# Optimization experiments

Hardware: AMD Instinct MI355X
Metric: run time of the kernel (lower is better)

Reference implementation:

```python
import jax, jax.numpy as jnp
import numpy as np

# ---- fixed problem dimensions ----
B, S, T = 64, 200, 32          # batch of sequences, trees per seq, nodes per tree
V, E, C = 50000, 128, 128      # vocab, embedding_dim, encode_dim
H, OUT = 100, 104              # GRU hidden, output_dim
N = B * S * T                  # total nodes
D_MAX = 5                      # max depth of a 32-node complete binary tree


def setup_inputs() -> dict:
    key = jax.random.key(0)
    ks = jax.random.split(key, 16)
    # --- tree structure: every tree is a complete binary tree with T nodes ---
    local_parent = np.array([0] + [(i - 1) // 2 for i in range(1, T)], dtype=np.int64)
    local_depth = np.array([int(np.floor(np.log2(i + 1))) for i in range(T)], dtype=np.int64)
    num_trees = B * S
    offsets = np.arange(num_trees, dtype=np.int64) * T
    node_parent = (offsets[:, None] + local_parent[None, :]).reshape(-1)
    node_depth = np.tile(local_depth, num_trees)
    node_tree = np.repeat(np.arange(num_trees, dtype=np.int64), T)
    node_tokens = jax.random.randint(ks[0], (N,), 0, V, dtype=jnp.int64)
    sc = 0.05
    inp = {
        "node_tokens": node_tokens,
        "node_parent": jnp.asarray(node_parent),
        "node_tree": jnp.asarray(node_tree),
        "node_depth": jnp.asarray(node_depth),
        "emb": jax.random.normal(ks[1], (V, E), jnp.float32) * sc,
        "w_lin": jax.random.normal(ks[2], (C, E), jnp.float32) * sc,
        "b_lin": jnp.zeros((C,), jnp.float32),
        "w_ih_f": jax.random.normal(ks[3], (3 * H, C), jnp.float32) * sc,
        "w_hh_f": jax.random.normal(ks[4], (3 * H, H), jnp.float32) * sc,
        "b_ih_f": jnp.zeros((3 * H,), jnp.float32),
        "b_hh_f": jnp.zeros((3 * H,), jnp.float32),
        "w_ih_b": jax.random.normal(ks[5], (3 * H, C), jnp.float32) * sc,
        "w_hh_b": jax.random.normal(ks[6], (3 * H, H), jnp.float32) * sc,
        "b_ih_b": jnp.zeros((3 * H,), jnp.float32),
        "b_hh_b": jnp.zeros((3 * H,), jnp.float32),
        "fc_w": jax.random.normal(ks[7], (OUT, 2 * H), jnp.float32) * sc,
        "fc_b": jnp.zeros((OUT,), jnp.float32),
    }
    return inp


def _gru(x_sbc, w_ih, w_hh, b_ih, b_hh):
    """Torch-convention GRU over leading time axis. x_sbc: [S, B, C] -> [S, B, H]."""
    h0 = jnp.zeros((x_sbc.shape[1], w_hh.shape[1]), x_sbc.dtype)

    def step(h, xt):
        gx = xt @ w_ih.T + b_ih
        gh = h @ w_hh.T + b_hh
        xr, xz, xn = jnp.split(gx, 3, axis=-1)
        hr, hz, hn = jnp.split(gh, 3, axis=-1)
        r = jax.nn.sigmoid(xr + hr)
        z = jax.nn.sigmoid(xz + hz)
        n = jnp.tanh(xn + r * hn)
        h_new = (1.0 - z) * n + z * h
        return h_new, h_new

    _, hs = jax.lax.scan(step, h0, x_sbc)
    return hs


def reference(node_tokens, node_parent, node_tree, node_depth,
              emb, w_lin, b_lin,
              w_ih_f, w_hh_f, b_ih_f, b_hh_f,
              w_ih_b, w_hh_b, b_ih_b, b_hh_b,
              fc_w, fc_b):
    # per-node contribution: W * emb(token) + b   (recursion base of hidden_state)
    c = emb[node_tokens] @ w_lin.T + b_lin               # [N, C]
    # level-batched bottom-up scatter-add: h(node) = c(node) + sum(h(children))
    h = c
    for d in range(D_MAX, 0, -1):
        mask = (node_depth == d)[:, None]
        h = h.at[node_parent].add(jnp.where(mask, h, 0.0))
    # per-tree max pool over all node hidden states (TreeEncoder output)
    tree_vec = jax.ops.segment_max(h, node_tree, num_segments=B * S)  # [B*S, C]
    x = tree_vec.reshape(B, S, C)
    # bidirectional GRU (batch_first in torch; scan over time here)
    x_t = jnp.transpose(x, (1, 0, 2))                    # [S, B, C]
    fwd = _gru(x_t, w_ih_f, w_hh_f, b_ih_f, b_hh_f)      # [S, B, H]
    bwd = _gru(x_t[::-1], w_ih_b, w_hh_b, b_ih_b, b_hh_b)[::-1]
    gru_out = jnp.concatenate([fwd, bwd], axis=-1)       # [S, B, 2H]
    pool = gru_out.max(axis=0)                           # [B, 2H] (max over time)
    return pool @ fc_w.T + fc_b                          # [B, OUT]
```

## Files before the change

kernel.cpp:

```cpp
#include <hip/hip_runtime.h>
#include <hip/hip_bf16.h>
#include <math.h>

#define BB 64
#define SS 200
#define TT 32
#define VV 50000
#define EE 128
#define CC 128
#define HH 100
#define G3 300
#define OUTD 104
#define NTREE (BB*SS)

typedef __attribute__((ext_vector_type(4))) float f32x4;
typedef _Float16 f16x8 __attribute__((ext_vector_type(8)));

#define L2E  1.4426950408889634f
#define NL2E (-1.4426950408889634f)
#define TL2E 2.8853900817779268f

#define BAR() asm volatile("s_waitcnt lgkmcnt(0)\n\ts_barrier" ::: "memory")


__global__ __launch_bounds__(256) void k0_prep(const float* __restrict__ w_lin,
                                               const float* __restrict__ w_ih_f,
                                               const float* __restrict__ w_ih_b,
                                               const float* __restrict__ w_hh_f,
                                               const float* __restrict__ w_hh_b,
                                               const float* __restrict__ emb,
                                               _Float16* __restrict__ wl,
                                               _Float16* __restrict__ k2b,
                                               _Float16* __restrict__ k3b,
                                               _Float16* __restrict__ emb16) {
    const int tid  = threadIdx.x;
    const int wave = tid >> 6;
    const int lane = tid & 63;
    const int r = lane & 15;
    const int q = lane >> 4;
    if (blockIdx.x == 0) {
#pragma unroll
        for (int nt = 0; nt < 2; ++nt)
#pragma unroll
            for (int kt = 0; kt < 4; ++kt) {
                const int n = wave * 32 + nt * 16 + r;
                const float* src = w_lin + (long)n * EE + kt * 32 + q * 8;
                f16x8 f;
#pragma unroll
                for (int e = 0; e < 8; ++e) f[e] = (_Float16)src[e];
                *(f16x8*)&wl[(size_t)((((wave * 2 + nt) * 4 + kt) * 64) + lane) * 8] = f;
            }
    } else if (blockIdx.x <= 10) {
        const int nb = blockIdx.x - 1;
        const int n = nb * 64 + wave * 16 + r;
        const int dir = (n >= 320) ? 1 : 0;
        const int j = n - dir * 320;
        const int jj = (j < G3) ? j : 0;
        const float* w = dir ? w_ih_b : w_ih_f;
#pragma unroll
        for (int kt = 0; kt < 4; ++kt) {
            const float* src = w + (long)jj * EE + kt * 32 + q * 8;
            f16x8 f;
#pragma unroll
            for (int e = 0; e < 8; ++e) f[e] = (_Float16)src[e];
            *(f16x8*)&k2b[(size_t)((((nb * 4 + wave) * 4 + kt) * 64) + lane) * 8] = f;
        }
    } else if (blockIdx.x <= 12) {
        const int d = blockIdx.x - 11;
        const float* whh = d ? w_hh_b : w_hh_f;
#pragma unroll
        for (int t = 0; t < 6; ++t) {
            const int gate = (t < 3) ? t : t - 3;
            const int ch   = (t < 3) ? r : 16 + r;
            const bool nv  = (ch < 25);
            const int row  = gate * HH + wave * 25 + (nv ? ch : 0);
            const float sc = (gate == 2) ? TL2E : NL2E;
#pragma unroll
            for (int kt = 0; kt < 4; ++kt) {
                f16x8 f;
#pragma unroll
                for (int e = 0; e < 8; ++e) {
                    const int k = kt * 32 + q * 8 + e;
                    f[e] = (_Float16)((nv && k < HH) ? sc * whh[row * HH + k] : 0.f);
                }
                *(f16x8*)&k3b[(size_t)((((d * 4 + wave) * 6 + t) * 4 + kt) * 64 + lane) * 8] = f;
            }
        }
    } else {
        const long base = (long)(blockIdx.x - 13) * 2048 + (long)tid * 8;
        if (base < (long)VV * EE) {
            const float4* s = (const float4*)(emb + base);
            const float4 v0 = s[0], v1 = s[1];
            f16x8 f;
            f[0] = (_Float16)v0.x; f[1] = (_Float16)v0.y;
            f[2] = (_Float16)v0.z; f[3] = (_Float16)v0.w;
            f[4] = (_Float16)v1.x; f[5] = (_Float16)v1.y;
            f[6] = (_Float16)v1.z; f[7] = (_Float16)v1.w;
            *(f16x8*)&emb16[base] = f;
        }
    }
}

#define K1_TPI 2
#define AROWS (K1_TPI*TT)
#define LDA 136
#define LDC 132

__global__ __launch_bounds__(256) void k1_mfma(const int* __restrict__ tok,
                                               const _Float16* __restrict__ emb16,
                                               const _Float16* __restrict__ wl,
                                               const float* __restrict__ b_lin,
                                               _Float16* __restrict__ thi) {
    __shared__ __align__(16) _Float16 A_sh[AROWS * LDA];
    __shared__ __align__(16) float C_sh[AROWS * LDC];
    __shared__ int tok_sh[AROWS];

    const int tid  = threadIdx.x;
    const int wave = tid >> 6;
    const int lane = tid & 63;
    const int r = lane & 15;
    const int q = lane >> 4;

    f16x8 bfrag[2][4];
    float bias[2];
#pragma unroll
    for (int nt = 0; nt < 2; ++nt) {
        bias[nt] = b_lin[wave * 32 + nt * 16 + r];
#pragma unroll
        for (int kt = 0; kt < 4; ++kt)
            bfrag[nt][kt] = *(const f16x8*)&wl[(size_t)((((wave * 2 + nt) * 4 + kt) * 64) + lane) * 8];
    }

    const int tree0 = blockIdx.x * K1_TPI;
    if (tid < AROWS) tok_sh[tid] = tok[tree0 * TT + tid];
    __syncthreads();

#pragma unroll
    for (int i = 0; i < 4; ++i) {
        const int idx = tid + i * 256;
        const int row = idx >> 4;
        const int p   = idx & 15;
        const f16x8 v = *(const f16x8*)&emb16[(long)tok_sh[row] * EE + p * 8];
        *(f16x8*)&A_sh[row * LDA + p * 8] = v;
    }
    __syncthreads();

    f32x4 acc[4][2];
#pragma unroll
    for (int mt = 0; mt < 4; ++mt)
#pragma unroll
        for (int nt = 0; nt < 2; ++nt) acc[mt][nt] = (f32x4)(0.f);

#pragma unroll
    for (int mt = 0; mt < 4; ++mt) {
        const int m = mt * 16 + r;
        f16x8 afrag[4];
#pragma unroll
        for (int kt = 0; kt < 4; ++kt)
            afrag[kt] = *(const f16x8*)&A_sh[m * LDA + kt * 32 + q * 8];
#pragma unroll
        for (int nt = 0; nt < 2; ++nt)
#pragma unroll
            for (int kt = 0; kt < 4; ++kt)
                acc[mt][nt] = __builtin_amdgcn_mfma_f32_16x16x32_f16(
                    afrag[kt], bfrag[nt][kt], acc[mt][nt], 0, 0, 0);
    }

#pragma unroll
    for (int mt = 0; mt < 4; ++mt)
#pragma unroll
        for (int nt = 0; nt < 2; ++nt) {
            const int col = wave * 32 + nt * 16 + r;
#pragma unroll
            for (int reg = 0; reg < 4; ++reg) {
                const int row = mt * 16 + q * 4 + reg;
                C_sh[row * LDC + col] = acc[mt][nt][reg] + bias[nt];
            }
        }
    __syncthreads();

    {
        const int t = tid >> 7;
        const int j = tid & 127;
        const float* base = &C_sh[(t * TT) * LDC + j];
        float v[TT];
#pragma unroll
        for (int n = 0; n < TT; ++n) v[n] = base[n * LDC];
        float mx = -1e30f;
#pragma unroll
        for (int n = TT - 1; n >= 1; --n) {
            mx = fmaxf(mx, v[n]);
            v[(n - 1) >> 1] += v[n];
        }
        mx = fmaxf(mx, v[0]);
        thi[(size_t)(tree0 + t) * CC + j] = (_Float16)mx;
    }
}

__global__ __launch_bounds__(256) void k2_mfma(const _Float16* __restrict__ thi,
                                               const _Float16* __restrict__ k2b,
                                               const float* __restrict__ b_ih_f,
                                               const float* __restrict__ b_ih_b,
                                               float* __restrict__ gx) {
    __shared__ __align__(16) _Float16 Ah[32 * LDA];

    const int tid  = threadIdx.x;
    const int wave = tid >> 6;
    const int lane = tid & 63;
    const int r = lane & 15;
    const int q = lane >> 4;

    const int nb = blockIdx.x % 10;
    const int mb = blockIdx.x / 10;
    const int m0 = mb * 32;
    const int n0 = nb * 64;

#pragma unroll
    for (int i = 0; i < 2; ++i) {
        const int idx = tid + i * 256;
        const int row = idx >> 4;
        const int p   = idx & 15;
        f16x8 v = *(const f16x8*)&thi[(size_t)(m0 + row) * CC + p * 8];
        *(f16x8*)&Ah[row * LDA + p * 8] = v;
    }
    f16x8 bh[4];
#pragma unroll
    for (int kt = 0; kt < 4; ++kt)
        bh[kt] = *(const f16x8*)&k2b[(size_t)((((nb * 4 + wave) * 4 + kt) * 64) + lane) * 8];
    __syncthreads();

    f32x4 acc[2];
    acc[0] = (f32x4)(0.f); acc[1] = (f32x4)(0.f);
#pragma unroll
    for (int mt = 0; mt < 2; ++mt) {
        const int m = mt * 16 + r;
#pragma unroll
        for (int kt = 0; kt < 4; ++kt) {
            f16x8 a = *(const f16x8*)&Ah[m * LDA + kt * 32 + q * 8];
            acc[mt] = __builtin_amdgcn_mfma_f32_16x16x32_f16(a, bh[kt], acc[mt], 0, 0, 0);
        }
    }

    const int ng  = n0 + wave * 16 + r;
    const int dir = (ng >= 320) ? 1 : 0;
    const int j   = ng - dir * 320;
    const bool valid = (j < G3);
    const float bias = valid ? (dir ? b_ih_b[j] : b_ih_f[j]) : 0.f;
    float* gxd = gx + (long)dir * NTREE * G3;
    if (valid) {
#pragma unroll
        for (int mt = 0; mt < 2; ++mt)
#pragma unroll
            for (int reg = 0; reg < 4; ++reg) {
                const int m = m0 + mt * 16 + q * 4 + reg;
                gxd[(long)m * G3 + j] = acc[mt][reg] + bias;
            }
    }
}

__global__ __launch_bounds__(256, 1) void k3_gru(const float* __restrict__ gx,
                                                 const _Float16* __restrict__ k3b,
                                                 const float* __restrict__ b_hh_f,
                                                 const float* __restrict__ b_hh_b,
                                                 float* __restrict__ pool) {
    const int bid = blockIdx.x;
    const int dir = bid & 1;
    const int b   = bid >> 1;
    const int tid = threadIdx.x;
    const int wave = tid >> 6;
    const int lane = tid & 63;
    const int r = lane & 15;
    const int q = lane >> 4;

    const float* b_hh = dir ? b_hh_b : b_hh_f;

    __shared__ __align__(16) _Float16 h_sh[2][128];

    const int dw = dir * 4 + wave;
    f16x8 bf[6][4];
#pragma unroll
    for (int t = 0; t < 6; ++t)
#pragma unroll
        for (int kt = 0; kt < 4; ++kt)
            bf[t][kt] = *(const f16x8*)&k3b[(size_t)(((dw * 6 + t) * 4 + kt) * 64 + lane) * 8];

    const int m = lane;
    const int c = wave * 25 + m;
    const bool act  = (m < 25);
    const bool lo16 = (m < 16);
    float brc = 0.f, bzc = 0.f, bnc = 0.f;
    if (act) {
        brc = NL2E * b_hh[c];
        bzc = NL2E * b_hh[HH + c];
        bnc = TL2E * b_hh[2 * HH + c];
    }

    if (tid < 128) { h_sh[0][tid] = (_Float16)0.f; h_sh[1][tid] = (_Float16)0.f; }

    const int sstep = dir ? -1 : 1;
    const int s0 = dir ? (SS - 1) : 0;
    const float* gp = gx + (long)dir * NTREE * G3 + (long)b * SS * G3 + c;

    float pxr[4], pxz[4], pxn[4];
    if (act) {
#pragma unroll
        for (int j = 0; j < 4; ++j) {
            const long off = (long)(s0 + j * sstep) * G3;
            pxr[j] = gp[off]; pxz[j] = gp[off + HH]; pxn[j] = gp[off + 2 * HH];
        }
    }
    float hj = 0.f, hmax = -1e30f;
    __syncthreads();

    int s = s0;
    for (int t0 = 0; t0 < SS; t0 += 4) {
#pragma unroll
        for (int j = 0; j < 4; ++j) {
            const int p = j & 1;

            f16x8 a[4];
#pragma unroll
            for (int kt = 0; kt < 4; ++kt)
                a[kt] = *(const f16x8*)&h_sh[p][kt * 32 + q * 8];

            const float xr = __builtin_fmaf(pxr[j], NL2E, brc);
            const float xz = __builtin_fmaf(pxz[j], NL2E, bzc);
            const float xn = pxn[j] * TL2E;

            f32x4 accA[6], accB[6];
#pragma unroll
            for (int i = 0; i < 6; ++i) {
                accA[i] = (f32x4)(0.f);
                accB[i] = (f32x4)(0.f);
                accA[i] = __builtin_amdgcn_mfma_f32_16x16x32_f16(a[0], bf[i][0], accA[i], 0, 0, 0);
                accB[i] = __builtin_amdgcn_mfma_f32_16x16x32_f16(a[2], bf[i][2], accB[i], 0, 0, 0);
                accA[i] = __builtin_amdgcn_mfma_f32_16x16x32_f16(a[1], bf[i][1], accA[i], 0, 0, 0);
                accB[i] = __builtin_amdgcn_mfma_f32_16x16x32_f16(a[3], bf[i][3], accB[i], 0, 0, 0);
            }
            const float G0 = accA[0][0] + accB[0][0];
            const float G1 = accA[1][0] + accB[1][0];
            const float G2 = accA[2][0] + accB[2][0];
            const float G3v = accA[3][0] + accB[3][0];
            const float G4 = accA[4][0] + accB[4][0];
            const float G5 = accA[5][0] + accB[5][0];
            const float ghr = lo16 ? G0 : G3v;
            const float ghz = lo16 ? G1 : G4;
            const float ghn = lo16 ? G2 : G5;

            if (act) {
                const float rg = __builtin_amdgcn_rcpf(1.f + __builtin_amdgcn_exp2f(xr + ghr));
                const float zg = __builtin_amdgcn_rcpf(1.f + __builtin_amdgcn_exp2f(xz + ghz));
                const float t1 = ghn + bnc;
                const float an = __builtin_fmaf(rg, t1, xn);
                const float u  = __builtin_amdgcn_rcpf(1.f + __builtin_amdgcn_exp2f(an));
                const float n  = __builtin_fmaf(-2.f, u, 1.f);
                hj = __builtin_fmaf(zg, hj - n, n);
                h_sh[1 - p][c] = (_Float16)hj;
                hmax = fmaxf(hmax, hj);
                if (t0 + j + 4 < SS) {
                    const long off = (long)(s + (j + 4) * sstep) * G3;
                    pxr[j] = gp[off]; pxz[j] = gp[off + HH]; pxn[j] = gp[off + 2 * HH];
                }
            }
            BAR();
        }
        s += 4 * sstep;
    }
    if (act) pool[(long)b * (2 * HH) + dir * HH + c] = hmax;
}

__global__ __launch_bounds__(256) void k4_fc(const float* __restrict__ pool,
                                             const float* __restrict__ fc_w,
                                             const float* __restrict__ fc_b,
                                             float* __restrict__ out) {
    const int b = blockIdx.x;
    __shared__ __align__(16) float p_sh[2 * HH];
    const int t = threadIdx.x;
    if (t < 2 * HH) p_sh[t] = pool[(long)b * (2 * HH) + t];
    __syncthreads();
    if (t < OUTD) {
        const float4* wr4 = (const float4*)(fc_w + (long)t * (2 * HH));
        const float4* p4 = (const float4*)p_sh;
        float a0 = 0.f, a1 = 0.f;
#pragma unroll
        for (int k = 0; k < 50; k += 2) {
            float4 w0 = wr4[k],   p0 = p4[k];
            float4 w1 = wr4[k+1], p1 = p4[k+1];
            a0 += w0.x*p0.x + w0.y*p0.y + w0.z*p0.z + w0.w*p0.w;
            a1 += w1.x*p1.x + w1.y*p1.y + w1.z*p1.z + w1.w*p1.w;
        }
        out[(long)b * OUTD + t] = fc_b[t] + a0 + a1;
    }
}

extern "C" void kernel_launch(void* const* d_in, const int* in_sizes, int n_in,
                              void* d_out, int out_size, void* d_ws, size_t ws_size,
                              hipStream_t stream) {
    const int*   tok    = (const int*)d_in[0];
    const float* emb    = (const float*)d_in[4];
    const float* w_lin  = (const float*)d_in[5];
    const float* b_lin  = (const float*)d_in[6];
    const float* w_ih_f = (const float*)d_in[7];
    const float* w_hh_f = (const float*)d_in[8];
    const float* b_ih_f = (const float*)d_in[9];
    const float* b_hh_f = (const float*)d_in[10];
    const float* w_ih_b = (const float*)d_in[11];
    const float* w_hh_b = (const float*)d_in[12];
    const float* b_ih_b = (const float*)d_in[13];
    const float* b_hh_b = (const float*)d_in[14];
    const float* fc_w   = (const float*)d_in[15];
    const float* fc_b   = (const float*)d_in[16];

    char* wsb = (char*)d_ws;
    _Float16* wl    = (_Float16*)(wsb);
    _Float16* k2b   = (_Float16*)(wsb + 32768);
    _Float16* thi   = (_Float16*)(wsb + 196608);
    _Float16* k3b   = (_Float16*)(wsb + 3473408);
    float*    gx    = (float*)(wsb + 3670016);
    _Float16* emb16 = (_Float16*)(wsb + 3670016);
    float*    pool  = (float*)(wsb);
    float*    out   = (float*)d_out;

    k0_prep<<<13 + 3125, 256, 0, stream>>>(w_lin, w_ih_f, w_ih_b, w_hh_f, w_hh_b, emb,
                                           wl, k2b, k3b, emb16);
    k1_mfma<<<NTREE / K1_TPI, 256, 0, stream>>>(tok, emb16, wl, b_lin, thi);
    k2_mfma<<<(NTREE / 32) * 10, 256, 0, stream>>>(thi, k2b, b_ih_f, b_ih_b, gx);
    k3_gru <<<2 * BB, 256, 0, stream>>>(gx, k3b, b_hh_f, b_hh_b, pool);
    k4_fc  <<<BB, 256, 0, stream>>>(pool, fc_w, fc_b, out);
}
```

Baseline: 252.5 us.

## Batch 16 sequences per GRU block so recurrent MFMAs use all rows

The GRU recurrence kernel previously ran one sequence per block (128 blocks), with each MFMA using only one of its 16 rows. It now processes 16 batch rows per block (8 blocks total), with the weights as the A operand and the hidden states of 16 sequences as the B operand, so each MFMA does useful work across all rows. The r/z hidden biases and the log2 scaling are folded into the gx projection kernel, and the LDS hidden-state buffer is XOR-swizzled. In exchange, far fewer CUs are occupied, and each of the 200 serial steps carries more MFMA and transcendental work per wave, so the latency-bound loop may lengthen.

```diff
diff --git a/kernel.cpp b/kernel.cpp
--- a/kernel.cpp
+++ b/kernel.cpp
@@ -15,6 +15,7 @@
 
 typedef __attribute__((ext_vector_type(4))) float f32x4;
 typedef _Float16 f16x8 __attribute__((ext_vector_type(8)));
+typedef _Float16 f16x4 __attribute__((ext_vector_type(4)));
 
 #define L2E  1.4426950408889634f
 #define NL2E (-1.4426950408889634f)
@@ -31,7 +32,7 @@
                                                const float* __restrict__ emb,
                                                _Float16* __restrict__ wl,
                                                _Float16* __restrict__ k2b,
-                                               _Float16* __restrict__ k3b,
+                                               _Float16* __restrict__ k3c,
                                                _Float16* __restrict__ emb16) {
     const int tid  = threadIdx.x;
     const int wave = tid >> 6;
@@ -68,23 +69,19 @@
     } else if (blockIdx.x <= 12) {
         const int d = blockIdx.x - 11;
         const float* whh = d ? w_hh_b : w_hh_f;
-#pragma unroll
-        for (int t = 0; t < 6; ++t) {
-            const int gate = (t < 3) ? t : t - 3;
-            const int ch   = (t < 3) ? r : 16 + r;
-            const bool nv  = (ch < 25);
-            const int row  = gate * HH + wave * 25 + (nv ? ch : 0);
-            const float sc = (gate == 2) ? TL2E : NL2E;
-#pragma unroll
-            for (int kt = 0; kt < 4; ++kt) {
-                f16x8 f;
-#pragma unroll
-                for (int e = 0; e < 8; ++e) {
-                    const int k = kt * 32 + q * 8 + e;
-                    f[e] = (_Float16)((nv && k < HH) ? sc * whh[row * HH + k] : 0.f);
-                }
-                *(f16x8*)&k3b[(size_t)((((d * 4 + wave) * 6 + t) * 4 + kt) * 64 + lane) * 8] = f;
-            }
+        for (int i = wave; i < 96; i += 4) {
+            const int cb = i / 12;
+            const int g  = (i % 12) / 4;
+            const int kt = i % 4;
+            const int ch = cb * 16 + r;
+            const float sc = (g == 2) ? TL2E : NL2E;
+            f16x8 f;
+#pragma unroll
+            for (int e = 0; e < 8; ++e) {
+                const int k = kt * 32 + q * 8 + e;
+                f[e] = (_Float16)((ch < HH && k < HH) ? sc * whh[(g * HH + ch) * HH + k] : 0.f);
+            }
+            *(f16x8*)&k3c[(size_t)((((d * 8 + cb) * 3 + g) * 4 + kt) * 64 + lane) * 8] = f;
         }
     } else {
         const long base = (long)(blockIdx.x - 13) * 2048 + (long)tid * 8;
@@ -201,6 +198,8 @@
                                                const _Float16* __restrict__ k2b,
                                                const float* __restrict__ b_ih_f,
                                                const float* __restrict__ b_ih_b,
+                                               const float* __restrict__ b_hh_f,
+                                               const float* __restrict__ b_hh_b,
                                                float* __restrict__ gx) {
     __shared__ __align__(16) _Float16 Ah[32 * LDA];
 
@@ -245,7 +244,11 @@
     const int dir = (ng >= 320) ? 1 : 0;
     const int j   = ng - dir * 320;
     const bool valid = (j < G3);
-    const float bias = valid ? (dir ? b_ih_b[j] : b_ih_f[j]) : 0.f;
+    const float* b_ih = dir ? b_ih_b : b_ih_f;
+    const float* b_hh = dir ? b_hh_b : b_hh_f;
+    const float bias = valid ? b_ih[j] : 0.f;
+    const float bh2  = (valid && j < 2 * HH) ? b_hh[j] : 0.f;
+    const float sc   = (j < 2 * HH) ? NL2E : TL2E;
     float* gxd = gx + (long)dir * NTREE * G3;
     if (valid) {
 #pragma unroll
@@ -253,120 +256,142 @@
 #pragma unroll
             for (int reg = 0; reg < 4; ++reg) {
                 const int m = m0 + mt * 16 + q * 4 + reg;
-                gxd[(long)m * G3 + j] = acc[mt][reg] + bias;
+                gxd[(long)m * G3 + j] = sc * (acc[mt][reg] + bias + bh2);
             }
     }
 }
 
 __global__ __launch_bounds__(256, 1) void k3_gru(const float* __restrict__ gx,
-                                                 const _Float16* __restrict__ k3b,
+                                                 const _Float16* __restrict__ k3c,
                                                  const float* __restrict__ b_hh_f,
                                                  const float* __restrict__ b_hh_b,
                                                  float* __restrict__ pool) {
     const int bid = blockIdx.x;
-    const int dir = bid & 1;
-    const int b   = bid >> 1;
+    const int dir = bid >> 2;
+    const int b0  = (bid & 3) * 16;
     const int tid = threadIdx.x;
     const int wave = tid >> 6;
     const int lane = tid & 63;
     const int r = lane & 15;
     const int q = lane >> 4;
+    const int rl3 = (r & 7) << 3;
 
     const float* b_hh = dir ? b_hh_b : b_hh_f;
 
-    __shared__ __align__(16) _Float16 h_sh[2][128];
-
-    const int dw = dir * 4 + wave;
-    f16x8 bf[6][4];
-#pragma unroll
-    for (int t = 0; t < 6; ++t)
-#pragma unroll
-        for (int kt = 0; kt < 4; ++kt)
-            bf[t][kt] = *(const f16x8*)&k3b[(size_t)(((dw * 6 + t) * 4 + kt) * 64 + lane) * 8];
-
-    const int m = lane;
-    const int c = wave * 25 + m;
-    const bool act  = (m < 25);
-    const bool lo16 = (m < 16);
-    float brc = 0.f, bzc = 0.f, bnc = 0.f;
-    if (act) {
-        brc = NL2E * b_hh[c];
-        bzc = NL2E * b_hh[HH + c];
-        bnc = TL2E * b_hh[2 * HH + c];
-    }
-
-    if (tid < 128) { h_sh[0][tid] = (_Float16)0.f; h_sh[1][tid] = (_Float16)0.f; }
+    __shared__ __align__(16) _Float16 h_sh[2][16][128];
+
+    f16x8 bf[2][3][4];
+#pragma unroll
+    for (int i = 0; i < 2; ++i) {
+        const int cb = wave * 2 + i;
+#pragma unroll
+        for (int g = 0; g < 3; ++g)
+#pragma unroll
+            for (int kt = 0; kt < 4; ++kt)
+                bf[i][g][kt] = *(const f16x8*)&k3c[(size_t)((((dir * 8 + cb) * 3 + g) * 4 + kt) * 64 + lane) * 8];
+    }
+
+    int  ch0[2]; bool vld[2]; int co[2][3];
+    f32x4 bnc[2];
+#pragma unroll
+    for (int i = 0; i < 2; ++i) {
+        const int cb = wave * 2 + i;
+        ch0[i] = cb * 16 + q * 4;
+        vld[i] = (ch0[i] < HH);
+#pragma unroll
+        for (int g = 0; g < 3; ++g) co[i][g] = vld[i] ? (g * HH + ch0[i]) : 0;
+        bnc[i] = (f32x4)(0.f);
+        if (vld[i]) {
+            const f32x4 bb = *(const f32x4*)&b_hh[2 * HH + ch0[i]];
+            bnc[i] = bb * TL2E;
+        }
+    }
+
+    ((f16x8*)h_sh)[tid] = (f16x8)(_Float16)0.f;
+    ((f16x8*)h_sh)[tid + 256] = (f16x8)(_Float16)0.f;
 
     const int sstep = dir ? -1 : 1;
     const int s0 = dir ? (SS - 1) : 0;
-    const float* gp = gx + (long)dir * NTREE * G3 + (long)b * SS * G3 + c;
-
-    float pxr[4], pxz[4], pxn[4];
-    if (act) {
-#pragma unroll
-        for (int j = 0; j < 4; ++j) {
-            const long off = (long)(s0 + j * sstep) * G3;
-            pxr[j] = gp[off]; pxz[j] = gp[off + HH]; pxn[j] = gp[off + 2 * HH];
-        }
-    }
-    float hj = 0.f, hmax = -1e30f;
-    __syncthreads();
-
-    int s = s0;
-    for (int t0 = 0; t0 < SS; t0 += 4) {
-#pragma unroll
-        for (int j = 0; j < 4; ++j) {
-            const int p = j & 1;
+    const float* gxd = gx + (long)dir * NTREE * G3;
+    const long rb = (long)(b0 + r) * SS;
+
+    f32x4 px[2][6];
+#pragma unroll
+    for (int j = 0; j < 2; ++j)
+#pragma unroll
+        for (int i = 0; i < 2; ++i)
+#pragma unroll
+            for (int g = 0; g < 3; ++g)
+                if (vld[i])
+                    px[j][i * 3 + g] = *(const f32x4*)(gxd + (rb + s0 + j * sstep) * G3 + co[i][g]);
+    const float* gpb = gxd + (rb + s0 + 2 * sstep) * G3;
+
+    f32x4 hs[2]   = {(f32x4)(0.f), (f32x4)(0.f)};
+    f32x4 hmax4[2] = {(f32x4)(-1e30f), (f32x4)(-1e30f)};
+    const f32x4 z4 = (f32x4)(0.f);
+    __syncthreads();
+
+    for (int t0 = 0; t0 < SS; t0 += 2) {
+#pragma unroll
+        for (int j = 0; j < 2; ++j) {
+            const int p = j;
 
             f16x8 a[4];
 #pragma unroll
             for (int kt = 0; kt < 4; ++kt)
-                a[kt] = *(const f16x8*)&h_sh[p][kt * 32 + q * 8];
-
-            const float xr = __builtin_fmaf(pxr[j], NL2E, brc);
-            const float xz = __builtin_fmaf(pxz[j], NL2E, bzc);
-            const float xn = pxn[j] * TL2E;
-
-            f32x4 accA[6], accB[6];
-#pragma unroll
-            for (int i = 0; i < 6; ++i) {
-                accA[i] = (f32x4)(0.f);
-                accB[i] = (f32x4)(0.f);
-                accA[i] = __builtin_amdgcn_mfma_f32_16x16x32_f16(a[0], bf[i][0], accA[i], 0, 0, 0);
-                accB[i] = __builtin_amdgcn_mfma_f32_16x16x32_f16(a[2], bf[i][2], accB[i], 0, 0, 0);
-                accA[i] = __builtin_amdgcn_mfma_f32_16x16x32_f16(a[1], bf[i][1], accA[i], 0, 0, 0);
-                accB[i] = __builtin_amdgcn_mfma_f32_16x16x32_f16(a[3], bf[i][3], accB[i], 0, 0, 0);
-            }
-            const float G0 = accA[0][0] + accB[0][0];
-            const float G1 = accA[1][0] + accB[1][0];
-            const float G2 = accA[2][0] + accB[2][0];
-            const float G3v = accA[3][0] + accB[3][0];
-            const float G4 = accA[4][0] + accB[4][0];
-            const float G5 = accA[5][0] + accB[5][0];
-            const float ghr = lo16 ? G0 : G3v;
-            const float ghz = lo16 ? G1 : G4;
-            const float ghn = lo16 ? G2 : G5;
-
-            if (act) {
-                const float rg = __builtin_amdgcn_rcpf(1.f + __builtin_amdgcn_exp2f(xr + ghr));
-                const float zg = __builtin_amdgcn_rcpf(1.f + __builtin_amdgcn_exp2f(xz + ghz));
-                const float t1 = ghn + bnc;
-                const float an = __builtin_fmaf(rg, t1, xn);
-                const float u  = __builtin_amdgcn_rcpf(1.f + __builtin_amdgcn_exp2f(an));
-                const float n  = __builtin_fmaf(-2.f, u, 1.f);
-                hj = __builtin_fmaf(zg, hj - n, n);
-                h_sh[1 - p][c] = (_Float16)hj;
-                hmax = fmaxf(hmax, hj);
-                if (t0 + j + 4 < SS) {
-                    const long off = (long)(s + (j + 4) * sstep) * G3;
-                    pxr[j] = gp[off]; pxz[j] = gp[off + HH]; pxn[j] = gp[off + 2 * HH];
+                a[kt] = *(const f16x8*)&h_sh[p][r][(kt * 32 + q * 8) ^ rl3];
+
+            f32x4 xv[6];
+#pragma unroll
+            for (int u = 0; u < 6; ++u) xv[u] = px[j][u];
+            if (t0 + j + 2 < SS) {
+#pragma unroll
+                for (int i = 0; i < 2; ++i)
+#pragma unroll
+                    for (int g = 0; g < 3; ++g)
+                        if (vld[i])
+                            px[j][i * 3 + g] = *(const f32x4*)(gpb + co[i][g]);
+            }
+            gpb += (long)sstep * G3;
+
+            f32x4 acc[2][3];
+#pragma unroll
+            for (int kt = 0; kt < 4; ++kt)
+#pragma unroll
+                for (int i = 0; i < 2; ++i)
+#pragma unroll
+                    for (int g = 0; g < 3; ++g)
+                        acc[i][g] = __builtin_amdgcn_mfma_f32_16x16x32_f16(
+                            bf[i][g][kt], a[kt], (kt == 0) ? z4 : acc[i][g], 0, 0, 0);
+
+#pragma unroll
+            for (int i = 0; i < 2; ++i) {
+#pragma unroll
+                for (int j2 = 0; j2 < 4; ++j2) {
+                    const float rg = __builtin_amdgcn_rcpf(1.f + __builtin_amdgcn_exp2f(xv[i * 3 + 0][j2] + acc[i][0][j2]));
+                    const float zg = __builtin_amdgcn_rcpf(1.f + __builtin_amdgcn_exp2f(xv[i * 3 + 1][j2] + acc[i][1][j2]));
+                    const float t1 = acc[i][2][j2] + bnc[i][j2];
+                    const float an = __builtin_fmaf(rg, t1, xv[i * 3 + 2][j2]);
+                    const float u  = __builtin_amdgcn_rcpf(1.f + __builtin_amdgcn_exp2f(an));
+                    const float nn = __builtin_fmaf(-2.f, u, 1.f);
+                    const float h  = __builtin_fmaf(zg, hs[i][j2] - nn, nn);
+                    hs[i][j2] = h;
+                    hmax4[i][j2] = fmaxf(hmax4[i][j2], h);
                 }
+                if (vld[i]) {
+                    f16x4 hv;
+#pragma unroll
+                    for (int j2 = 0; j2 < 4; ++j2) hv[j2] = (_Float16)hs[i][j2];
+                    *(f16x4*)&h_sh[1 - p][r][ch0[i] ^ rl3] = hv;
+                }
             }
             BAR();
         }
-        s += 4 * sstep;
-    }
-    if (act) pool[(long)b * (2 * HH) + dir * HH + c] = hmax;
+    }
+#pragma unroll
+    for (int i = 0; i < 2; ++i)
+        if (vld[i])
+            *(f32x4*)&pool[(long)(b0 + r) * (2 * HH) + dir * HH + ch0[i]] = hmax4[i];
 }
 
 __global__ __launch_bounds__(256) void k4_fc(const float* __restrict__ pool,
@@ -415,16 +440,17 @@
     _Float16* wl    = (_Float16*)(wsb);
     _Float16* k2b   = (_Float16*)(wsb + 32768);
     _Float16* thi   = (_Float16*)(wsb + 196608);
-    _Float16* k3b   = (_Float16*)(wsb + 3473408);
+    _Float16* k3c   = (_Float16*)(wsb + 3473408);
     float*    gx    = (float*)(wsb + 3670016);
     _Float16* emb16 = (_Float16*)(wsb + 3670016);
     float*    pool  = (float*)(wsb);
     float*    out   = (float*)d_out;
 
     k0_prep<<<13 + 3125, 256, 0, stream>>>(w_lin, w_ih_f, w_ih_b, w_hh_f, w_hh_b, emb,
-                                           wl, k2b, k3b, emb16);
+                                           wl, k2b, k3c, emb16);
     k1_mfma<<<NTREE / K1_TPI, 256, 0, stream>>>(tok, emb16, wl, b_lin, thi);
-    k2_mfma<<<(NTREE / 32) * 10, 256, 0, stream>>>(thi, k2b, b_ih_f, b_ih_b, gx);
-    k3_gru <<<2 * BB, 256, 0, stream>>>(gx, k3b, b_hh_f, b_hh_b, pool);
+    k2_mfma<<<(NTREE / 32) * 10, 256, 0, stream>>>(thi, k2b, b_ih_f, b_ih_b,
+                                                   b_hh_f, b_hh_b, gx);
+    k3_gru <<<8, 256, 0, stream>>>(gx, k3c, b_hh_f, b_hh_b, pool);
     k4_fc  <<<BB, 256, 0, stream>>>(pool, fc_w, fc_b, out);
 }
```

Measured after the change: 330.8 us. +31.0%, slower.
